# Performance work log

Hardware: AMD Instinct MI355X
Metric: run time of the kernel (lower is better)

The kernel has to match this reference:

```python
import jax, jax.numpy as jnp
import numpy as np

B, H, W, DIM = 8, 96, 96, 384
HEADS, HD = 12, 32
WS = 12
DISP = WS // 2
NWH, NWW = H // WS, W // WS
NW = NWH * NWW
INNER = HEADS * HD
NEG = float('-inf')


def _create_mask(ws, d, upper_lower, left_right):
    m = np.zeros((ws * ws, ws * ws), np.float32)
    if upper_lower:
        m[-d * ws:, :-d * ws] = NEG
        m[:-d * ws, -d * ws:] = NEG
    if left_right:
        m4 = m.reshape(ws, ws, ws, ws)
        m4[:, -d:, :, :-d] = NEG
        m4[:, :-d, :, -d:] = NEG
        m = m4.reshape(ws * ws, ws * ws)
    return m


def _rel_indices(ws):
    ind = np.array([[x, y] for x in range(ws) for y in range(ws)])
    return ind[None, :, :] - ind[:, None, :] + ws - 1  # [ws^2, ws^2, 2]


_UL = _create_mask(WS, DISP, True, False)
_LR = _create_mask(WS, DISP, False, True)
_WM = np.zeros((NW, WS * WS, WS * WS), np.float32)
_WM[-NWW:] += _UL            # last row of windows: upper/lower mask
_WM[NWW - 1::NWW] += _LR     # last column of windows: left/right mask
WMASK = jnp.asarray(_WM)
RI = _rel_indices(WS)  # static numpy indices


def _to_windows(t):
    # [B, H, W, INNER] -> [B, HEADS, NW, WS*WS, HD]
    b = t.shape[0]
    t = t.reshape(b, NWH, WS, NWW, WS, HEADS, HD)
    t = t.transpose(0, 5, 1, 3, 2, 4, 6)
    return t.reshape(b, HEADS, NW, WS * WS, HD)


def setup_inputs() -> dict:
    key = jax.random.key(0)
    ks = jax.random.split(key, 7)
    x = jax.random.normal(ks[0], (B, H, W, DIM), jnp.float32)
    pix_map = jax.random.randint(ks[1], (B, H, W), 0, 2, jnp.int32)
    w_qkv = jax.random.normal(ks[2], (DIM, 3 * INNER), jnp.float32) * (DIM ** -0.5)
    pos_embedding = jax.random.normal(ks[3], (2 * WS - 1, 2 * WS - 1), jnp.float32)
    pix_embedding = jax.random.normal(ks[4], (2,), jnp.float32)
    w_out = jax.random.normal(ks[5], (INNER, DIM), jnp.float32) * (INNER ** -0.5)
    b_out = jnp.zeros((DIM,), jnp.float32)
    return dict(x=x, pix_map=pix_map, w_qkv=w_qkv, pos_embedding=pos_embedding,
                pix_embedding=pix_embedding, w_out=w_out, b_out=b_out)


def reference(x, pix_map, w_qkv, pos_embedding, pix_embedding, w_out, b_out):
    scale = HD ** -0.5
    xs = jnp.roll(x, (-DISP, -DISP), (1, 2))  # cyclic shift
    qkv = xs @ w_qkv
    q, k, v = jnp.split(qkv, 3, axis=-1)
    q, k, v = _to_windows(q), _to_windows(k), _to_windows(v)
    dots = jnp.einsum('bhwid,bhwjd->bhwij', q, k) * scale  # [B,HEADS,NW,144,144]
    # dynamic pixel-map mask (note: original does NOT shift pix_map)
    pm = pix_map.astype(dots.dtype).reshape(-1, NWH, WS, NWW, WS)
    pm = pm.transpose(0, 1, 3, 2, 4).reshape(-1, NW, WS * WS)  # [B,NW,144]
    prod = pm[:, :, :, None] * pm[:, :, None, :]  # [B,NW,144,144]
    pix_mask = jnp.where(prod == 0, pix_embedding[0],
                         jnp.where(prod == 1, pix_embedding[1], prod))
    dots = dots + pix_mask[:, None]
    # relative position bias
    dots = dots + pos_embedding[RI[:, :, 0], RI[:, :, 1]]
    # shifted-window masks
    dots = dots + WMASK[None, None]
    attn = jax.nn.softmax(dots, axis=-1)
    out = jnp.einsum('bhwij,bhwjd->bhwid', attn, v)
    b = out.shape[0]
    out = out.reshape(b, HEADS, NWH, NWW, WS, WS, HD)
    out = out.transpose(0, 2, 4, 3, 5, 1, 6).reshape(b, H, W, INNER)
    out = out @ w_out + b_out
    return jnp.roll(out, (DISP, DISP), (1, 2))  # cyclic back shift
```

## Files before the change

kernel.cpp:

```cpp
#include <hip/hip_runtime.h>
#include <hip/hip_bf16.h>

#define BB 8
#define HH 96
#define WW2 96
#define DIM 384
#define HEADS 12
#define HD 32
#define WS 12
#define DISP 6
#define NWH 8
#define NWW 8
#define NW 64
#define TPW 144
#define INNER 384
#define NQKV 1152
#define MTOK (BB*NW*TPW)
#define SCALE 0.17677669529663687f

typedef short short8_t __attribute__((ext_vector_type(8)));
typedef float float4_t __attribute__((ext_vector_type(4)));
typedef unsigned short ushort8_t __attribute__((ext_vector_type(8)));
typedef unsigned short ushort4_t __attribute__((ext_vector_type(4)));

__device__ __forceinline__ float us2f(unsigned short u) {
    union { unsigned int u32; float f; } c; c.u32 = ((unsigned int)u) << 16; return c.f;
}
__device__ __forceinline__ unsigned short f2us(float f) {
    union { float f; unsigned int u; } c; c.f = f;
    unsigned int u = c.u;
    u += 0x7FFFu + ((u >> 16) & 1u);
    return (unsigned short)(u >> 16);
}

__global__ __launch_bounds__(256) void cast_wqkvT(
    const float* __restrict__ wqkv, unsigned short* __restrict__ wqkvT)
{
    int idx = blockIdx.x * 256 + threadIdx.x;
    if (idx >= NQKV * DIM) return;
    int n = idx / DIM, k = idx - n * DIM;
    wqkvT[idx] = f2us(wqkv[k * NQKV + n]);
}

__global__ __launch_bounds__(256, 2) void fused_attn(
    const float* __restrict__ x,
    const unsigned short* __restrict__ wqkvT,
    const int* __restrict__ pix_map,
    const float* __restrict__ pos_emb,
    const float* __restrict__ pix_emb,
    unsigned short* __restrict__ ao)
{
    __shared__ float qs[TPW][HD + 1];
    __shared__ float ks[TPW][HD + 1];
    __shared__ unsigned short vt[HD][168];
    __align__(16) __shared__ char uni[23552];
    __shared__ float pos[529];
    __shared__ int   pmv[TPW];
    __shared__ int   rowoff[TPW];

    unsigned short* xw  = (unsigned short*)uni;
    unsigned short* wcT = (unsigned short*)(uni + 11520);

    const int tid = threadIdx.x;
    const int w = blockIdx.x, h = blockIdx.y, b = blockIdx.z;
    const int nwy = w >> 3, nww = w & 7;
    const int tbase = (b * NW + w) * TPW;

    if (tid < TPW) {
        int ri = tid / WS, ci = tid - ri * WS;
        int ys = nwy * WS + ri, xs2 = nww * WS + ci;
        int yin = ys + DISP; if (yin >= HH) yin -= HH;
        int xin = xs2 + DISP; if (xin >= WW2) xin -= WW2;
        rowoff[tid] = ((b * HH + yin) * WW2 + xin) * DIM;
        pmv[tid] = pix_map[(b * HH + ys) * WW2 + xs2];
    }
    for (int idx = tid; idx < 529; idx += 256) pos[idx] = pos_emb[idx];
    {
        int zr = tid >> 3, zc = tid & 7;
        *(unsigned int*)(&vt[zr][144 + zc * 2]) = 0u;
    }
    __syncthreads();

    const int wave = tid >> 6, lane = tid & 63;
    const int quad = lane >> 4, l16 = lane & 15;
    const int mw = wave >> 1, nw = wave & 1;
    const int nmt = mw ? 4 : 5;
    const int mbase = mw * 5, nbase = nw * 3;

    float4_t acc[5][3];
    #pragma unroll
    for (int i = 0; i < 5; i++)
        #pragma unroll
        for (int j = 0; j < 3; j++) acc[i][j] = (float4_t){0.f, 0.f, 0.f, 0.f};

    for (int k0 = 0; k0 < DIM; k0 += 32) {
        for (int idx = tid; idx < 576; idx += 256) {
            int r = idx >> 2, qr = idx & 3;
            const float* src = x + rowoff[r] + k0 + qr * 8;
            float4 a = *(const float4*)src;
            float4 c = *(const float4*)(src + 4);
            ushort8_t u;
            u[0] = f2us(a.x); u[1] = f2us(a.y); u[2] = f2us(a.z); u[3] = f2us(a.w);
            u[4] = f2us(c.x); u[5] = f2us(c.y); u[6] = f2us(c.z); u[7] = f2us(c.w);
            *(ushort8_t*)(xw + r * 40 + qr * 8) = u;
        }
        for (int idx = tid; idx < 384; idx += 256) {
            int r = idx >> 2, c = (idx & 3) << 3;
            int s = r >> 5, nn = r & 31;
            int gn = s * INNER + h * HD + nn;
            *(ushort8_t*)(wcT + r * 40 + c) =
                *(const ushort8_t*)(wqkvT + gn * DIM + k0 + c);
        }
        __syncthreads();
        short8_t afr[5], bfr[3];
        #pragma unroll
        for (int j = 0; j < 3; j++)
            bfr[j] = *(short8_t*)(wcT + ((nbase + j) * 16 + l16) * 40 + quad * 8);
        #pragma unroll
        for (int i = 0; i < 5; i++)
            if (i < nmt)
                afr[i] = *(short8_t*)(xw + ((mbase + i) * 16 + l16) * 40 + quad * 8);
        #pragma unroll
        for (int i = 0; i < 5; i++)
            if (i < nmt)
                #pragma unroll
                for (int j = 0; j < 3; j++)
                    acc[i][j] = __builtin_amdgcn_mfma_f32_16x16x32_bf16(
                        afr[i], bfr[j], acc[i][j], 0, 0, 0);
        __syncthreads();
    }
    #pragma unroll
    for (int i = 0; i < 5; i++)
        if (i < nmt) {
            int tm = mbase + i;
            #pragma unroll
            for (int j = 0; j < 3; j++) {
                int tn = nbase + j;
                int s = tn >> 1;
                int cc = ((tn & 1) << 4) | l16;
                if (s == 2) {
                    ushort4_t pk;
                    #pragma unroll
                    for (int r = 0; r < 4; r++) pk[r] = f2us(acc[i][j][r]);
                    *(ushort4_t*)(&vt[cc][tm * 16 + quad * 4]) = pk;
                } else {
                    float* dst = (s == 0) ? &qs[0][0] : &ks[0][0];
                    float mul = (s == 0) ? SCALE : 1.0f;
                    #pragma unroll
                    for (int r = 0; r < 4; r++)
                        dst[(tm * 16 + quad * 4 + r) * (HD + 1) + cc] = acc[i][j][r] * mul;
                }
            }
        }
    __syncthreads();

    unsigned short* pscr = (unsigned short*)uni + wave * (16 * 184);
    {
        int zr = lane >> 2, zc = lane & 3;
        *(unsigned long long*)(pscr + zr * 184 + 144 + zc * 4) = 0ULL;
    }
    const float pe0 = pix_emb[0], pe1 = pix_emb[1];
    const bool ul = (nwy == NWH - 1), lr = (nww == NWW - 1);
    const int mt_start = wave ? (wave * 2 + 1) : 0;
    const int mt_count = wave ? 2 : 3;

    for (int it = 0; it < mt_count; ++it) {
        const int mt = mt_start + it;
        short8_t qh, ql;
        {
            const float* qrow = &qs[mt * 16 + l16][quad * 8];
            #pragma unroll
            for (int j2 = 0; j2 < 8; j2++) {
                float f = qrow[j2];
                unsigned short hh = f2us(f);
                qh[j2] = (short)hh;
                ql[j2] = (short)f2us(f - us2f(hh));
            }
        }
        float4_t s[9];
        #pragma unroll
        for (int nt = 0; nt < 9; nt++) {
            const float* krow = &ks[nt * 16 + l16][quad * 8];
            short8_t kh, kl;
            #pragma unroll
            for (int j2 = 0; j2 < 8; j2++) {
                float f = krow[j2];
                unsigned short hh = f2us(f);
                kh[j2] = (short)hh;
                kl[j2] = (short)f2us(f - us2f(hh));
            }
            float4_t a = (float4_t){0.f, 0.f, 0.f, 0.f};
            a = __builtin_amdgcn_mfma_f32_16x16x32_bf16(qh, kh, a, 0, 0, 0);
            a = __builtin_amdgcn_mfma_f32_16x16x32_bf16(ql, kh, a, 0, 0, 0);
            a = __builtin_amdgcn_mfma_f32_16x16x32_bf16(qh, kl, a, 0, 0, 0);
            s[nt] = a;
        }
        const int ib = mt * 16 + quad * 4;
        int riA[4], ciA[4], pmA[4];
        float mx[4];
        #pragma unroll
        for (int r = 0; r < 4; r++) {
            int i = ib + r;
            riA[r] = i / 12; ciA[r] = i - riA[r] * 12;
            pmA[r] = pmv[i];
            mx[r] = -3e38f;
        }
        #pragma unroll
        for (int nt = 0; nt < 9; nt++) {
            int j = nt * 16 + l16;
            int rj = j / 12, cj = j - rj * 12;
            int pj = pmv[j];
            bool jul = (rj >= 6), jlr = (cj >= 6);
            #pragma unroll
            for (int r = 0; r < 4; r++) {
                float a = s[nt][r];
                a += pos[(rj - riA[r] + 11) * 23 + (cj - ciA[r] + 11)];
                a += (pmA[r] * pj) ? pe1 : pe0;
                if (ul && ((riA[r] >= 6) != jul)) a -= 1e30f;
                if (lr && ((ciA[r] >= 6) != jlr)) a -= 1e30f;
                s[nt][r] = a;
                mx[r] = fmaxf(mx[r], a);
            }
        }
        #pragma unroll
        for (int r = 0; r < 4; r++) {
            float m2 = mx[r];
            m2 = fmaxf(m2, __shfl_xor(m2, 1));
            m2 = fmaxf(m2, __shfl_xor(m2, 2));
            m2 = fmaxf(m2, __shfl_xor(m2, 4));
            m2 = fmaxf(m2, __shfl_xor(m2, 8));
            mx[r] = m2;
        }
        float sm[4] = {0.f, 0.f, 0.f, 0.f};
        #pragma unroll
        for (int nt = 0; nt < 9; nt++)
            #pragma unroll
            for (int r = 0; r < 4; r++) {
                float e = __expf(s[nt][r] - mx[r]);
                s[nt][r] = e;
                sm[r] += e;
            }
        #pragma unroll
        for (int r = 0; r < 4; r++) {
            float s2 = sm[r];
            s2 += __shfl_xor(s2, 1); s2 += __shfl_xor(s2, 2);
            s2 += __shfl_xor(s2, 4); s2 += __shfl_xor(s2, 8);
            sm[r] = 1.0f / s2;
        }
        #pragma unroll
        for (int nt = 0; nt < 9; nt++)
            #pragma unroll
            for (int r = 0; r < 4; r++) {
                float p = s[nt][r] * sm[r];
                unsigned short hh = f2us(p);
                s[nt][r] = p - us2f(hh);
                pscr[(quad * 4 + r) * 184 + nt * 16 + l16] = hh;
            }
        float4_t o0 = (float4_t){0.f, 0.f, 0.f, 0.f};
        float4_t o1 = (float4_t){0.f, 0.f, 0.f, 0.f};
        #pragma unroll
        for (int ks2 = 0; ks2 < 5; ks2++) {
            short8_t pa = *(short8_t*)(pscr + l16 * 184 + ks2 * 32 + quad * 8);
            short8_t v0 = *(short8_t*)(&vt[l16][ks2 * 32 + quad * 8]);
            short8_t v1 = *(short8_t*)(&vt[16 + l16][ks2 * 32 + quad * 8]);
            o0 = __builtin_amdgcn_mfma_f32_16x16x32_bf16(pa, v0, o0, 0, 0, 0);
            o1 = __builtin_amdgcn_mfma_f32_16x16x32_bf16(pa, v1, o1, 0, 0, 0);
        }
        #pragma unroll
        for (int nt = 0; nt < 9; nt++)
            #pragma unroll
            for (int r = 0; r < 4; r++)
                pscr[(quad * 4 + r) * 184 + nt * 16 + l16] = f2us(s[nt][r]);
        #pragma unroll
        for (int ks2 = 0; ks2 < 5; ks2++) {
            short8_t pa = *(short8_t*)(pscr + l16 * 184 + ks2 * 32 + quad * 8);
            short8_t v0 = *(short8_t*)(&vt[l16][ks2 * 32 + quad * 8]);
            short8_t v1 = *(short8_t*)(&vt[16 + l16][ks2 * 32 + quad * 8]);
            o0 = __builtin_amdgcn_mfma_f32_16x16x32_bf16(pa, v0, o0, 0, 0, 0);
            o1 = __builtin_amdgcn_mfma_f32_16x16x32_bf16(pa, v1, o1, 0, 0, 0);
        }
        size_t obase = (size_t)(tbase + mt * 16 + quad * 4) * INNER + h * HD;
        #pragma unroll
        for (int r = 0; r < 4; r++) {
            ao[obase + (size_t)r * INNER + l16]      = f2us(o0[r]);
            ao[obase + (size_t)r * INNER + 16 + l16] = f2us(o1[r]);
        }
    }
}

#define TM 64
#define TN 64
#define TK 32

__global__ __launch_bounds__(256) void proj_gemm(
    const unsigned short* __restrict__ ao,
    const float* __restrict__ wout,
    const float* __restrict__ bout,
    float* __restrict__ out)
{
    __shared__ float As[TK][TM];
    __shared__ float Bs[TK][TN];
    __shared__ int rowoff[TM];
    const int tid = threadIdx.x;
    const int n0 = blockIdx.x * TN;
    const int m0 = blockIdx.y * TM;
    if (tid < TM) {
        int t = m0 + tid;
        int b = t / (NW * TPW);
        int r = t - b * (NW * TPW);
        int w = r / TPW;
        int i = r - w * TPW;
        int nwy = w >> 3, nww = w & 7;
        int ri = i / WS, ci = i - ri * WS;
        int ys = nwy * WS + ri, xs = nww * WS + ci;
        int yo = ys + DISP; if (yo >= HH) yo -= HH;
        int xo = xs + DISP; if (xo >= WW2) xo -= WW2;
        rowoff[tid] = ((b * HH + yo) * WW2 + xo) * DIM;
    }
    __syncthreads();
    const int tx = tid & 15, ty = tid >> 4;
    const int am = tid >> 2, ad = (tid & 3) << 3;
    const int bk = tid >> 3, bn = (tid & 7) << 3;
    float acc[4][4] = {};
    for (int k0 = 0; k0 < INNER; k0 += TK) {
        ushort8_t a8 = *(const ushort8_t*)(ao + (size_t)(m0 + am) * INNER + k0 + ad);
        float4 b0 = *(const float4*)(wout + (k0 + bk) * DIM + n0 + bn);
        float4 b1 = *(const float4*)(wout + (k0 + bk) * DIM + n0 + bn + 4);
        #pragma unroll
        for (int j = 0; j < 8; j++) As[ad + j][am] = us2f(a8[j]);
        *(float4*)&Bs[bk][bn]     = b0;
        *(float4*)&Bs[bk][bn + 4] = b1;
        __syncthreads();
        #pragma unroll
        for (int kk = 0; kk < TK; kk++) {
            float4 a = *(const float4*)&As[kk][ty * 4];
            float4 b = *(const float4*)&Bs[kk][tx * 4];
            float av[4] = {a.x, a.y, a.z, a.w};
            float bv[4] = {b.x, b.y, b.z, b.w};
            #pragma unroll
            for (int ii = 0; ii < 4; ii++)
                #pragma unroll
                for (int jj = 0; jj < 4; jj++)
                    acc[ii][jj] += av[ii] * bv[jj];
        }
        __syncthreads();
    }
    float4 bo = *(const float4*)(bout + n0 + tx * 4);
    #pragma unroll
    for (int ii = 0; ii < 4; ii++) {
        float4 r;
        r.x = acc[ii][0] + bo.x;
        r.y = acc[ii][1] + bo.y;
        r.z = acc[ii][2] + bo.z;
        r.w = acc[ii][3] + bo.w;
        *(float4*)(out + (size_t)rowoff[ty * 4 + ii] + n0 + tx * 4) = r;
    }
}

extern "C" void kernel_launch(void* const* d_in, const int* in_sizes, int n_in,
                              void* d_out, int out_size, void* d_ws, size_t ws_size,
                              hipStream_t stream) {
    const float* x       = (const float*)d_in[0];
    const int*   pix_map = (const int*)d_in[1];
    const float* wqkv    = (const float*)d_in[2];
    const float* pos_emb = (const float*)d_in[3];
    const float* pix_emb = (const float*)d_in[4];
    const float* wout    = (const float*)d_in[5];
    const float* bout    = (const float*)d_in[6];
    float* out = (float*)d_out;

    unsigned short* ao     = (unsigned short*)d_ws;
    unsigned short* wqkvT  = ao + (size_t)MTOK * INNER;

    cast_wqkvT<<<(NQKV * DIM + 255) / 256, 256, 0, stream>>>(wqkv, wqkvT);

    dim3 g2(NW, HEADS, BB);
    fused_attn<<<g2, 256, 0, stream>>>(x, wqkvT, pix_map, pos_emb, pix_emb, ao);

    dim3 g3(DIM / TN, MTOK / TM);
    proj_gemm<<<g3, 256, 0, stream>>>(ao, wout, bout, out);
}
```

Measured before the change: 913.7 us.

## Replace FP32 output projection GEMM with bf16 MFMA using split-weight precision

```diff
diff --git a/kernel.cpp b/kernel.cpp
--- a/kernel.cpp
+++ b/kernel.cpp
@@ -288,23 +288,20 @@
     }
 }
 
-#define TM 64
-#define TN 64
-#define TK 32
-
-__global__ __launch_bounds__(256) void proj_gemm(
+__global__ __launch_bounds__(256) void proj_mfma(
     const unsigned short* __restrict__ ao,
     const float* __restrict__ wout,
     const float* __restrict__ bout,
     float* __restrict__ out)
 {
-    __shared__ float As[TK][TM];
-    __shared__ float Bs[TK][TN];
-    __shared__ int rowoff[TM];
+    __align__(16) __shared__ unsigned short As[128 * 40];
+    __align__(16) __shared__ unsigned short Bh[64 * 40];
+    __align__(16) __shared__ unsigned short Bl[64 * 40];
+    __shared__ int rowoff[128];
     const int tid = threadIdx.x;
-    const int n0 = blockIdx.x * TN;
-    const int m0 = blockIdx.y * TM;
-    if (tid < TM) {
+    const int n0 = blockIdx.x * 64;
+    const int m0 = blockIdx.y * 128;
+    if (tid < 128) {
         int t = m0 + tid;
         int b = t / (NW * TPW);
         int r = t - b * (NW * TPW);
@@ -318,43 +315,63 @@
         rowoff[tid] = ((b * HH + yo) * WW2 + xo) * DIM;
     }
     __syncthreads();
-    const int tx = tid & 15, ty = tid >> 4;
-    const int am = tid >> 2, ad = (tid & 3) << 3;
-    const int bk = tid >> 3, bn = (tid & 7) << 3;
-    float acc[4][4] = {};
-    for (int k0 = 0; k0 < INNER; k0 += TK) {
-        ushort8_t a8 = *(const ushort8_t*)(ao + (size_t)(m0 + am) * INNER + k0 + ad);
-        float4 b0 = *(const float4*)(wout + (k0 + bk) * DIM + n0 + bn);
-        float4 b1 = *(const float4*)(wout + (k0 + bk) * DIM + n0 + bn + 4);
-        #pragma unroll
-        for (int j = 0; j < 8; j++) As[ad + j][am] = us2f(a8[j]);
-        *(float4*)&Bs[bk][bn]     = b0;
-        *(float4*)&Bs[bk][bn + 4] = b1;
+    const int wave = tid >> 6, lane = tid & 63;
+    const int quad = lane >> 4, l16 = lane & 15;
+    const int mw = wave >> 1, nw2 = wave & 1;
+    const int bn = tid & 63;
+    const int bkb = (tid >> 6) * 8;
+
+    float4_t acc[4][2];
+    #pragma unroll
+    for (int i = 0; i < 4; i++)
+        #pragma unroll
+        for (int j = 0; j < 2; j++) acc[i][j] = (float4_t){0.f, 0.f, 0.f, 0.f};
+
+    for (int k0 = 0; k0 < INNER; k0 += 32) {
+        for (int idx = tid; idx < 512; idx += 256) {
+            int r = idx >> 2, c = (idx & 3) << 3;
+            *(ushort8_t*)(As + r * 40 + c) =
+                *(const ushort8_t*)(ao + (size_t)(m0 + r) * INNER + k0 + c);
+        }
+        #pragma unroll
+        for (int j = 0; j < 8; j++) {
+            float v = wout[(size_t)(k0 + bkb + j) * DIM + n0 + bn];
+            unsigned short hi = f2us(v);
+            Bh[bn * 40 + bkb + j] = hi;
+            Bl[bn * 40 + bkb + j] = f2us(v - us2f(hi));
+        }
         __syncthreads();
-        #pragma unroll
-        for (int kk = 0; kk < TK; kk++) {
-            float4 a = *(const float4*)&As[kk][ty * 4];
-            float4 b = *(const float4*)&Bs[kk][tx * 4];
-            float av[4] = {a.x, a.y, a.z, a.w};
-            float bv[4] = {b.x, b.y, b.z, b.w};
-            #pragma unroll
-            for (int ii = 0; ii < 4; ii++)
-                #pragma unroll
-                for (int jj = 0; jj < 4; jj++)
-                    acc[ii][jj] += av[ii] * bv[jj];
-        }
+        short8_t af[4], bhf[2], blf[2];
+        #pragma unroll
+        for (int nt = 0; nt < 2; nt++) {
+            bhf[nt] = *(short8_t*)(Bh + (nw2 * 32 + nt * 16 + l16) * 40 + quad * 8);
+            blf[nt] = *(short8_t*)(Bl + (nw2 * 32 + nt * 16 + l16) * 40 + quad * 8);
+        }
+        #pragma unroll
+        for (int mt = 0; mt < 4; mt++)
+            af[mt] = *(short8_t*)(As + (mw * 64 + mt * 16 + l16) * 40 + quad * 8);
+        #pragma unroll
+        for (int mt = 0; mt < 4; mt++)
+            #pragma unroll
+            for (int nt = 0; nt < 2; nt++) {
+                acc[mt][nt] = __builtin_amdgcn_mfma_f32_16x16x32_bf16(
+                    af[mt], bhf[nt], acc[mt][nt], 0, 0, 0);
+                acc[mt][nt] = __builtin_amdgcn_mfma_f32_16x16x32_bf16(
+                    af[mt], blf[nt], acc[mt][nt], 0, 0, 0);
+            }
         __syncthreads();
     }
-    float4 bo = *(const float4*)(bout + n0 + tx * 4);
+    float bo0 = bout[n0 + nw2 * 32 + l16];
+    float bo1 = bout[n0 + nw2 * 32 + 16 + l16];
     #pragma unroll
-    for (int ii = 0; ii < 4; ii++) {
-        float4 r;
-        r.x = acc[ii][0] + bo.x;
-        r.y = acc[ii][1] + bo.y;
-        r.z = acc[ii][2] + bo.z;
-        r.w = acc[ii][3] + bo.w;
-        *(float4*)(out + (size_t)rowoff[ty * 4 + ii] + n0 + tx * 4) = r;
-    }
+    for (int mt = 0; mt < 4; mt++)
+        #pragma unroll
+        for (int r = 0; r < 4; r++) {
+            int ml = mw * 64 + mt * 16 + quad * 4 + r;
+            size_t rb = (size_t)rowoff[ml] + n0 + nw2 * 32;
+            out[rb + l16]      = acc[mt][0][r] + bo0;
+            out[rb + 16 + l16] = acc[mt][1][r] + bo1;
+        }
 }
 
 extern "C" void kernel_launch(void* const* d_in, const int* in_sizes, int n_in,
@@ -377,6 +394,6 @@
     dim3 g2(NW, HEADS, BB);
     fused_attn<<<g2, 256, 0, stream>>>(x, wqkvT, pix_map, pos_emb, pix_emb, ao);
 
-    dim3 g3(DIM / TN, MTOK / TM);
-    proj_gemm<<<g3, 256, 0, stream>>>(ao, wout, bout, out);
-}
+    dim3 g3(DIM / 64, MTOK / 128);
+    proj_mfma<<<g3, 256, 0, stream>>>(ao, wout, bout, out);
+}
```

Result: faster. 746.2 us (-18.3%).
